# Performance work log

Hardware: AMD Instinct MI355X
Metric: run time of the kernel (lower is better)

The kernel has to match this reference:

```python
import jax, jax.numpy as jnp
import numpy as np

IN_C, OUT_C, K, STRIDE = 128, 256, 3, 1

def setup_inputs() -> dict:
    key = jax.random.key(0)
    k1, k2 = jax.random.split(key)
    x = jax.random.normal(k1, (32, IN_C, 112, 112), dtype=jnp.float32)
    weight = jax.random.normal(k2, (OUT_C, IN_C, K, K), dtype=jnp.float32)
    bias = jnp.zeros((OUT_C,), dtype=jnp.float32)
    return {"x": x, "weight": weight, "bias": bias}

def reference(x, weight, bias):
    # valid-padding direct conv, NCHW / OIHW layout, stride STRIDE
    out = jax.lax.conv_general_dilated(
        x, weight,
        window_strides=(STRIDE, STRIDE),
        padding='VALID',
        dimension_numbers=('NCHW', 'OIHW', 'NCHW'))
    return out + bias[None, :, None, None]
```

## Files before the change

kernel.cpp:

```cpp
#include <hip/hip_runtime.h>

#define NI 32
#define CI 128
#define HI 112
#define WI 112
#define OC 256
#define HO 110
#define WO 110

typedef float f32x4 __attribute__((ext_vector_type(4)));
typedef short s16x8 __attribute__((ext_vector_type(8)));

typedef const unsigned int __attribute__((address_space(1))) gu32;
typedef unsigned int __attribute__((address_space(3))) lu32;

__device__ __forceinline__ ushort f2bf(float f) {
  union { float f; unsigned int u; } x; x.f = f;
  unsigned int r = x.u + 0x7FFFu + ((x.u >> 16) & 1u);
  return (ushort)(r >> 16);
}

__global__ __launch_bounds__(256) void pack_w_kernel(const float* __restrict__ w,
                                                     ushort* __restrict__ wp) {
  int i = blockIdx.x * 256 + threadIdx.x;
  int e = i & 7;
  int k8 = (i >> 3) & 3;
  int oc = (i >> 5) & 255;
  int cq = (i >> 13) & 3;
  int kk = i >> 15;
  int ch = cq * 32 + k8 * 8 + e;
  int kh = kk / 3, kw = kk - kh * 3;
  wp[i] = f2bf(w[((oc * CI + ch) * 3 + kh) * 3 + kw]);
}

__global__ __launch_bounds__(256) void to_nhwc_kernel(const float* __restrict__ x,
                                                      ushort* __restrict__ xn) {
  __shared__ ushort lds[1792 * 8];
  int b = blockIdx.x;
  int n = b / HI;
  int h = b - n * HI;
  const float* xr = x + ((size_t)n * CI * HI) * WI + (size_t)h * WI;
  int t = threadIdx.x;
  int w = t & 127;
  int cph = t >> 7;
  if (w < WI) {
    #pragma unroll
    for (int it = 0; it < 32; ++it) {
      int cp = it * 2 + cph;
      int c = cp * 2;
      float f0 = xr[(size_t)c * (HI * WI) + w];
      float f1 = xr[(size_t)(c + 1) * (HI * WI) + w];
      unsigned int pk = (unsigned int)f2bf(f0) | ((unsigned int)f2bf(f1) << 16);
      int chunk = w * 16 + ((cp >> 2) ^ (w & 15));
      *(unsigned int*)((char*)lds + chunk * 16 + (cp & 3) * 4) = pk;
    }
  }
  __syncthreads();
  #pragma unroll
  for (int it = 0; it < 7; ++it) {
    int j = it * 256 + t;
    int w2 = j >> 4, c8 = j & 15;
    int src = w2 * 16 + (c8 ^ (w2 & 15));
    uint4 v = *(const uint4*)((const char*)lds + src * 16);
    int cq = c8 >> 2, g = c8 & 3;
    *(uint4*)&xn[((((size_t)n * 4 + cq) * HI + h) * WI + w2) * 32 + g * 8] = v;
  }
}

__global__ __launch_bounds__(256, 2) void conv_mfma_kernel(const ushort* __restrict__ xn,
                                                           const ushort* __restrict__ wp,
                                                           const float* __restrict__ bias,
                                                           float* __restrict__ out) {
  __shared__ ushort lds[2 * 340 * 32];
  const int bid = blockIdx.x;
  const int orig = (bid & 7) * 440 + (bid >> 3);
  const int n = orig / HO;
  const int oh = orig - n * HO;
  const int t = threadIdx.x;
  const int lane = t & 63;
  const int wid = t >> 6;
  const int lane15 = lane & 15;
  const int laneh = lane >> 4;
  const int oc0 = wid * 64;
  char* ldsb = (char*)lds;

  f32x4 acc[4][7] = {};
  s16x8 abuf[4][4];

#define A_PREFETCH(gg)                                                                   \
  {                                                                                      \
    const int q_ = (gg) / 9, kk_ = (gg) - q_ * 9;                                        \
    const ushort* wb_ = wp + ((size_t)(kk_ * 4 + q_)) * 8192 + (oc0 + lane15) * 32 +     \
                        laneh * 8;                                                       \
    _Pragma("unroll") for (int mf = 0; mf < 4; ++mf)                                     \
        abuf[(gg) & 3][mf] = *(const s16x8*)(wb_ + mf * 512);                            \
  }

#define STAGE(qq)                                                                        \
  {                                                                                      \
    const char* gsb_ =                                                                   \
        (const char*)(xn + ((((size_t)n * 4 + (qq)) * HI + oh) * WI) * 32);              \
    char* ldst_ = ldsb + (((qq) & 1) * 21760);                                           \
    _Pragma("unroll") for (int i = 0; i < 6; ++i) {                                      \
      int idx = i * 256 + t;                                                             \
      if (idx < 1344) {                                                                  \
        int L = idx * 16;                                                                \
        int go = L ^ (((L >> 7) & 3) << 4);                                              \
        __builtin_amdgcn_global_load_lds((gu32*)(gsb_ + go), (lu32*)(ldst_ + L), 16, 0,  \
                                         0);                                             \
      }                                                                                  \
    }                                                                                    \
  }

  A_PREFETCH(0)
  A_PREFETCH(1)
  A_PREFETCH(2)
  STAGE(0)
  __syncthreads();

  #pragma unroll
  for (int q = 0; q < 4; ++q) {
    if (q) __syncthreads();
    if (q < 3) STAGE(q + 1)
    const int qb = (q & 1) * 21760;
    #pragma unroll
    for (int kk = 0; kk < 9; ++kk) {
      const int g = q * 9 + kk;
      const int kh = kk / 3, kw = kk - kh * 3;
      if (g + 3 < 36) A_PREFETCH(g + 3)
      s16x8 b[7];
      #pragma unroll
      for (int nf = 0; nf < 7; ++nf) {
        int R = kh * WI + nf * 16 + lane15 + kw;
        int addr = qb + (R << 6) + ((laneh ^ ((R >> 1) & 3)) << 4);
        b[nf] = *(const s16x8*)(ldsb + addr);
      }
      __builtin_amdgcn_s_setprio(1);
      #pragma unroll
      for (int mf = 0; mf < 4; ++mf)
        #pragma unroll
        for (int nf = 0; nf < 7; ++nf)
          acc[mf][nf] = __builtin_amdgcn_mfma_f32_16x16x32_bf16(abuf[g & 3][mf], b[nf],
                                                                acc[mf][nf], 0, 0, 0);
      __builtin_amdgcn_s_setprio(0);
    }
  }
#undef A_PREFETCH
#undef STAGE

  float* outb = out + ((size_t)n * OC) * (HO * WO) + (size_t)oh * WO;
  #pragma unroll
  for (int mf = 0; mf < 4; ++mf) {
    #pragma unroll
    for (int r = 0; r < 4; ++r) {
      const int oc = oc0 + mf * 16 + laneh * 4 + r;
      const float bv = bias[oc];
      float* op = outb + (size_t)oc * (HO * WO);
      #pragma unroll
      for (int nf = 0; nf < 7; ++nf) {
        int ow = nf * 16 + lane15;
        if (ow < WO) op[ow] = acc[mf][nf][r] + bv;
      }
    }
  }
}

__global__ __launch_bounds__(256) void conv_naive_kernel(const float* __restrict__ x,
                                                         const float* __restrict__ w,
                                                         const float* __restrict__ bias,
                                                         float* __restrict__ out) {
  long i = (long)blockIdx.x * 256 + threadIdx.x;
  const long total = (long)NI * OC * HO * WO;
  if (i >= total) return;
  int ow = (int)(i % WO);
  long r1 = i / WO;
  int oh = (int)(r1 % HO);
  long r2 = r1 / HO;
  int oc = (int)(r2 % OC);
  int n = (int)(r2 / OC);
  float s = bias[oc];
  const float* xb = x + ((size_t)n * CI * HI) * WI;
  const float* wb = w + (size_t)oc * CI * 9;
  for (int c = 0; c < CI; ++c)
    for (int kh = 0; kh < 3; ++kh)
      for (int kw = 0; kw < 3; ++kw)
        s += xb[((size_t)c * HI + oh + kh) * WI + ow + kw] * wb[(c * 3 + kh) * 3 + kw];
  out[i] = s;
}

extern "C" void kernel_launch(void* const* d_in, const int* in_sizes, int n_in,
                              void* d_out, int out_size, void* d_ws, size_t ws_size,
                              hipStream_t stream) {
  const float* x = (const float*)d_in[0];
  const float* w = (const float*)d_in[1];
  const float* bias = (const float*)d_in[2];
  float* out = (float*)d_out;

  const size_t xn_elems = (size_t)NI * 4 * HI * WI * 32;
  const size_t wp_elems = (size_t)9 * 4 * 256 * 32;
  const size_t need = (xn_elems + wp_elems) * sizeof(ushort);

  if (ws_size >= need) {
    ushort* xnw = (ushort*)d_ws;
    ushort* wpw = xnw + xn_elems;
    hipLaunchKernelGGL(pack_w_kernel, dim3((unsigned)(wp_elems / 256)), dim3(256), 0, stream,
                       w, wpw);
    hipLaunchKernelGGL(to_nhwc_kernel, dim3(NI * HI), dim3(256), 0, stream, x, xnw);
    hipLaunchKernelGGL(conv_mfma_kernel, dim3(NI * HO), dim3(256), 0, stream, xnw, wpw, bias,
                       out);
  } else {
    long total = (long)NI * OC * HO * WO;
    hipLaunchKernelGGL(conv_naive_kernel, dim3((unsigned)((total + 255) / 256)), dim3(256), 0,
                       stream, x, w, bias, out);
  }
}
```

Measured before the change: 362.8 us.

## Split output channels across two blocks and double-buffer LDS B-fragment loads

Each block now covers half of the output channels (128 instead of 256), so the grid doubles and each wave holds a 32x112 accumulator tile. The smaller register footprint allows three blocks per CU. B fragments are software-pipelined from LDS one kernel tap ahead, and A prefetch depth drops to one tap. The next channel-quarter stage is issued mid-loop. In exchange, every input row is staged into LDS twice (once per channel half), and each LDS B read now feeds fewer MFMAs.

Measured after the change: 333.5 us. 1.09x faster.

```diff
diff --git a/kernel.cpp b/kernel.cpp
--- a/kernel.cpp
+++ b/kernel.cpp
@@ -67,33 +67,47 @@
   }
 }
 
-__global__ __launch_bounds__(256, 2) void conv_mfma_kernel(const ushort* __restrict__ xn,
+__global__ __launch_bounds__(256, 3) void conv_mfma_kernel(const ushort* __restrict__ xn,
                                                            const ushort* __restrict__ wp,
                                                            const float* __restrict__ bias,
                                                            float* __restrict__ out) {
   __shared__ ushort lds[2 * 340 * 32];
   const int bid = blockIdx.x;
-  const int orig = (bid & 7) * 440 + (bid >> 3);
-  const int n = orig / HO;
-  const int oh = orig - n * HO;
+  const int orig = (bid & 7) * 880 + (bid >> 3);
+  const int p = orig >> 1;
+  const int och = orig & 1;
+  const int n = p / HO;
+  const int oh = p - n * HO;
   const int t = threadIdx.x;
   const int lane = t & 63;
   const int wid = t >> 6;
   const int lane15 = lane & 15;
   const int laneh = lane >> 4;
-  const int oc0 = wid * 64;
+  const int ocb = och * 128 + wid * 32;
   char* ldsb = (char*)lds;
 
-  f32x4 acc[4][7] = {};
-  s16x8 abuf[4][4];
-
-#define A_PREFETCH(gg)                                                                   \
+  f32x4 acc[2][7] = {};
+  s16x8 abuf[2][2];
+  s16x8 bbuf[2][7];
+
+#define A_PRE(gg)                                                                        \
   {                                                                                      \
     const int q_ = (gg) / 9, kk_ = (gg) - q_ * 9;                                        \
-    const ushort* wb_ = wp + ((size_t)(kk_ * 4 + q_)) * 8192 + (oc0 + lane15) * 32 +     \
+    const ushort* wb_ = wp + ((size_t)(kk_ * 4 + q_)) * 8192 + (ocb + lane15) * 32 +     \
                         laneh * 8;                                                       \
-    _Pragma("unroll") for (int mf = 0; mf < 4; ++mf)                                     \
-        abuf[(gg) & 3][mf] = *(const s16x8*)(wb_ + mf * 512);                            \
+    _Pragma("unroll") for (int mf = 0; mf < 2; ++mf)                                     \
+        abuf[(gg) & 1][mf] = *(const s16x8*)(wb_ + mf * 512);                            \
+  }
+
+#define B_PRE(qq, kk_, par)                                                              \
+  {                                                                                      \
+    const int kh_ = (kk_) / 3, kw_ = (kk_) - kh_ * 3;                                    \
+    const int qb_ = ((qq) & 1) * 21760;                                                  \
+    _Pragma("unroll") for (int nf = 0; nf < 7; ++nf) {                                   \
+      int R = kh_ * WI + nf * 16 + lane15 + kw_;                                         \
+      int addr = qb_ + (R << 6) + ((laneh ^ ((R >> 1) & 3)) << 4);                       \
+      bbuf[par][nf] = *(const s16x8*)(ldsb + addr);                                      \
+    }                                                                                    \
   }
 
 #define STAGE(qq)                                                                        \
@@ -112,48 +126,43 @@
     }                                                                                    \
   }
 
-  A_PREFETCH(0)
-  A_PREFETCH(1)
-  A_PREFETCH(2)
+  A_PRE(0)
   STAGE(0)
   __syncthreads();
+  B_PRE(0, 0, 0)
 
   #pragma unroll
   for (int q = 0; q < 4; ++q) {
-    if (q) __syncthreads();
-    if (q < 3) STAGE(q + 1)
-    const int qb = (q & 1) * 21760;
+    if (q) {
+      __syncthreads();
+      B_PRE(q, 0, (q * 9) & 1)
+    }
     #pragma unroll
     for (int kk = 0; kk < 9; ++kk) {
       const int g = q * 9 + kk;
-      const int kh = kk / 3, kw = kk - kh * 3;
-      if (g + 3 < 36) A_PREFETCH(g + 3)
-      s16x8 b[7];
-      #pragma unroll
-      for (int nf = 0; nf < 7; ++nf) {
-        int R = kh * WI + nf * 16 + lane15 + kw;
-        int addr = qb + (R << 6) + ((laneh ^ ((R >> 1) & 3)) << 4);
-        b[nf] = *(const s16x8*)(ldsb + addr);
-      }
+      if (g + 1 < 36) A_PRE(g + 1)
+      if (kk < 8) B_PRE(q, kk + 1, (g + 1) & 1)
+      if (kk == 1 && q < 3) STAGE(q + 1)
       __builtin_amdgcn_s_setprio(1);
       #pragma unroll
-      for (int mf = 0; mf < 4; ++mf)
+      for (int nf = 0; nf < 7; ++nf)
         #pragma unroll
-        for (int nf = 0; nf < 7; ++nf)
-          acc[mf][nf] = __builtin_amdgcn_mfma_f32_16x16x32_bf16(abuf[g & 3][mf], b[nf],
-                                                                acc[mf][nf], 0, 0, 0);
+        for (int mf = 0; mf < 2; ++mf)
+          acc[mf][nf] = __builtin_amdgcn_mfma_f32_16x16x32_bf16(
+              abuf[g & 1][mf], bbuf[g & 1][nf], acc[mf][nf], 0, 0, 0);
       __builtin_amdgcn_s_setprio(0);
     }
   }
-#undef A_PREFETCH
+#undef A_PRE
+#undef B_PRE
 #undef STAGE
 
   float* outb = out + ((size_t)n * OC) * (HO * WO) + (size_t)oh * WO;
   #pragma unroll
-  for (int mf = 0; mf < 4; ++mf) {
+  for (int mf = 0; mf < 2; ++mf) {
     #pragma unroll
     for (int r = 0; r < 4; ++r) {
-      const int oc = oc0 + mf * 16 + laneh * 4 + r;
+      const int oc = ocb + mf * 16 + laneh * 4 + r;
       const float bv = bias[oc];
       float* op = outb + (size_t)oc * (HO * WO);
       #pragma unroll
@@ -206,8 +215,8 @@
     hipLaunchKernelGGL(pack_w_kernel, dim3((unsigned)(wp_elems / 256)), dim3(256), 0, stream,
                        w, wpw);
     hipLaunchKernelGGL(to_nhwc_kernel, dim3(NI * HI), dim3(256), 0, stream, x, xnw);
-    hipLaunchKernelGGL(conv_mfma_kernel, dim3(NI * HO), dim3(256), 0, stream, xnw, wpw, bias,
-                       out);
+    hipLaunchKernelGGL(conv_mfma_kernel, dim3(NI * HO * 2), dim3(256), 0, stream, xnw, wpw,
+                       bias, out);
   } else {
     long total = (long)NI * OC * HO * WO;
     hipLaunchKernelGGL(conv_naive_kernel, dim3((unsigned)((total + 255) / 256)), dim3(256), 0,
```
